# Optimization experiments

Hardware: AMD Instinct MI355X
Metric: run time of the kernel (lower is better)

Reference implementation:

```python
import jax, jax.numpy as jnp
import numpy as np

K_HOP = 2

def _graph_conv(x, A, W, b):
    feats = [x]
    xk = x
    for _ in range(K_HOP):
        xk = jnp.einsum('bmn,bnc->bmc', A, xk)
        feats.append(xk)
    return jnp.concatenate(feats, -1) @ W + b

def _pair_mlp(y, W2, b2, W1, b1, shape):
    # normal_conv: fc1(relu(fc2(y))).reshape(shape)
    return (jax.nn.relu(y @ W2 + b2) @ W1 + b1).reshape(shape)

def setup_inputs():
    key = jax.random.key(0)
    ks = jax.random.split(key, 16)
    B, T, N = 8, 12, 200
    C_IN, H, D, H_ST = 2, 64, 32, 64
    def lin(k, fi, fo):
        k1, k2 = jax.random.split(k)
        s = 1.0 / float(np.sqrt(fi))
        return (jax.random.uniform(k1, (fi, fo), jnp.float32, -s, s),
                jax.random.uniform(k2, (fo,), jnp.float32, -s, s))
    W_s2d, b_s2d = lin(ks[0], H_ST, D)
    W_rz, b_rz = lin(ks[1], 1 + D, 2 * D)
    W_h, b_h = lin(ks[2], 1 + D, D)
    Wc2, bc2 = lin(ks[3], 2 * D, D)
    Wc1, bc1 = lin(ks[4], D, 1)
    Wm2, bm2 = lin(ks[5], 2 * D, D)
    Wm1, bm1 = lin(ks[6], D, 1)
    gin = (C_IN + H) * (1 + K_HOP)
    W_ru, b_ru = lin(ks[7], gin, 2 * H)
    W_cand, b_cand = lin(ks[8], gin, H)
    Wp1, bp1 = lin(ks[9], H, H)
    Wp2, bp2 = lin(ks[10], H, 1)
    x = jax.random.normal(ks[11], (B, T, N, C_IN), jnp.float32)
    node_fea_st = jax.random.normal(ks[12], (N, H_ST), jnp.float32)
    return dict(x=x, node_fea_st=node_fea_st, W_s2d=W_s2d, b_s2d=b_s2d,
                W_rz=W_rz, b_rz=b_rz, W_h=W_h, b_h=b_h,
                Wc2=Wc2, bc2=bc2, Wc1=Wc1, bc1=bc1,
                Wm2=Wm2, bm2=bm2, Wm1=Wm1, bm1=bm1,
                W_ru=W_ru, b_ru=b_ru, W_cand=W_cand, b_cand=b_cand,
                Wp1=Wp1, bp1=bp1, Wp2=Wp2, bp2=bp2)

def reference(x, node_fea_st, W_s2d, b_s2d, W_rz, b_rz, W_h, b_h,
              Wc2, bc2, Wc1, bc1, Wm2, bm2, Wm1, bm1,
              W_ru, b_ru, W_cand, b_cand, Wp1, bp1, Wp2, bp2):
    B, T, N, _ = x.shape
    H = W_cand.shape[1]
    D = W_h.shape[1]
    # states_dy init: linear_s2d(node_fea_st) broadcast over batch
    state_dy0 = jnp.broadcast_to((node_fea_st @ W_s2d + b_s2d)[None], (B, N, D))
    state0 = jnp.zeros((B, N, H), x.dtype)
    xs = jnp.transpose(x, (1, 0, 2, 3))  # [T,B,N,C]

    def step(carry, xt):
        state, state_dy = carry
        inp1 = xt[..., :1]
        # DynamicGraphGRU (conv_method='normal')
        rz = jax.nn.sigmoid(jnp.concatenate([inp1, state_dy], -1) @ W_rz + b_rz)
        r, z = jnp.split(rz, 2, -1)
        h = jnp.tanh(jnp.concatenate([inp1, r * state_dy], -1) @ W_h + b_h)
        new_dy = z * state_dy + (1.0 - z) * h
        s = jax.nn.relu(new_dy)  # [B,N,D]
        y = jnp.concatenate([jnp.broadcast_to(s[:, :, None, :], (B, N, N, D)),
                             jnp.broadcast_to(s[:, None, :, :], (B, N, N, D))], -1)
        g = _pair_mlp(y, Wc2, bc2, Wc1, bc1, (B, N, N))
        m = _pair_mlp(y, Wm2, bm2, Wm1, bm1, (B, N, N))
        A = g * jax.nn.sigmoid(m)  # dynamic graph [B,N,N]
        # DCGRUCell with supports=[A]
        ru = jax.nn.sigmoid(_graph_conv(jnp.concatenate([xt, state], -1), A, W_ru, b_ru))
        rr, u = jnp.split(ru, 2, -1)
        c = jnp.tanh(_graph_conv(jnp.concatenate([xt, rr * state], -1), A, W_cand, b_cand))
        new_state = u * state + (1.0 - u) * c
        return (new_state, new_dy), A

    (state, _), dy_graphs = jax.lax.scan(step, (state0, state_dy0), xs)
    # predictor: Linear -> LeakyReLU -> Linear
    pred = jax.nn.leaky_relu(state @ Wp1 + bp1) @ Wp2 + bp2  # [B,N,1]
    return pred, dy_graphs
```

## Files before the change

kernel.cpp:

```cpp
#include <hip/hip_runtime.h>
#include <math.h>

#define B_ 8
#define T_ 12
#define N_ 200
#define R_ 1600
#define NN_ 40000

__device__ __forceinline__ float sigm(float v) { return 1.f / (1.f + expf(-v)); }

__global__ void __launch_bounds__(256) k_dyall(
        const float* __restrict__ x,  const float* __restrict__ nf,
        const float* __restrict__ Ws2d, const float* __restrict__ bs2d,
        const float* __restrict__ Wrz,  const float* __restrict__ brz,
        const float* __restrict__ Wh,   const float* __restrict__ bh,
        const float* __restrict__ Wc2,  const float* __restrict__ Wm2,
        const float* __restrict__ bc2,  const float* __restrict__ bm2,
        float* __restrict__ Pc, float* __restrict__ Qc,
        float* __restrict__ Pm, float* __restrict__ Qm,
        float* __restrict__ state) {
    __shared__ float sWs2d[64 * 32], sWrz[33 * 64], sWh[33 * 32];
    __shared__ float sWc2[64 * 32], sWm2[64 * 32];
    __shared__ float sbrz[64], sbh[32], sbs2d[32], sbc2[32], sbm2[32];
    __shared__ float nfs[4][64], dy[4][32], in1[4][33], in2[4][33], rz[4][64], s4[4][32];
    int bk = blockIdx.x, tid = threadIdx.x;
    int w = tid >> 6, o = tid & 63;
    int row = bk * 4 + w, b = row / N_, n = row % N_;
    state[bk * 256 + tid] = 0.f;
    for (int idx = tid; idx < 2048; idx += 256) sWs2d[idx] = Ws2d[idx];
    for (int idx = tid; idx < 2112; idx += 256) sWrz[idx] = Wrz[idx];
    for (int idx = tid; idx < 1056; idx += 256) sWh[idx] = Wh[idx];
    for (int idx = tid; idx < 2048; idx += 256) { sWc2[idx] = Wc2[idx]; sWm2[idx] = Wm2[idx]; }
    if (tid < 64) sbrz[tid] = brz[tid];
    if (tid < 32) { sbh[tid] = bh[tid]; sbs2d[tid] = bs2d[tid];
                    sbc2[tid] = bc2[tid]; sbm2[tid] = bm2[tid]; }
    nfs[w][o] = nf[n * 64 + o];
    __syncthreads();
    if (o < 32) {
        float acc = sbs2d[o];
        #pragma unroll 8
        for (int i = 0; i < 64; ++i) acc += nfs[w][i] * sWs2d[i * 32 + o];
        dy[w][o] = acc;
    }
    __syncthreads();
    for (int t = 0; t < T_; ++t) {
        if (o == 0) { float v = x[((b * T_ + t) * N_ + n) * 2]; in1[w][0] = v; in2[w][0] = v; }
        if (o < 32) in1[w][o + 1] = dy[w][o];
        __syncthreads();
        float acc = sbrz[o];
        #pragma unroll
        for (int i = 0; i < 33; ++i) acc += in1[w][i] * sWrz[i * 64 + o];
        rz[w][o] = sigm(acc);
        __syncthreads();
        if (o < 32) in2[w][o + 1] = rz[w][o] * dy[w][o];
        __syncthreads();
        if (o < 32) {
            float h = sbh[o];
            #pragma unroll
            for (int i = 0; i < 33; ++i) h += in2[w][i] * sWh[i * 32 + o];
            h = tanhf(h);
            float z = rz[w][32 + o];
            float nd = z * dy[w][o] + (1.f - z) * h;
            dy[w][o] = nd;
            s4[w][o] = nd > 0.f ? nd : 0.f;
        }
        __syncthreads();
        size_t base = ((size_t)t * R_ + row) * 32;
        for (int idx = o; idx < 128; idx += 64) {
            int mat = idx >> 5, k = idx & 31;
            const float* W = (mat < 2) ? sWc2 : sWm2;
            int rb = (mat & 1) ? 32 : 0;
            float a = (mat == 0) ? sbc2[k] : (mat == 2) ? sbm2[k] : 0.f;
            #pragma unroll
            for (int i = 0; i < 32; ++i) a += s4[w][i] * W[(rb + i) * 32 + k];
            ((mat == 0) ? Pc : (mat == 1) ? Qc : (mat == 2) ? Pm : Qm)[base + k] = a;
        }
        __syncthreads();
    }
}

__global__ void __launch_bounds__(256) k_pairall(
        const float* __restrict__ Pc, const float* __restrict__ Qc,
        const float* __restrict__ Pm, const float* __restrict__ Qm,
        const float* __restrict__ Wc1, const float* __restrict__ bc1,
        const float* __restrict__ Wm1, const float* __restrict__ bm1,
        float* __restrict__ out) {
    __shared__ float sPc[16][36], sQc[16][36], sPm[16][36], sQm[16][36];
    __shared__ float sWc1[32], sWm1[32];
    int z = blockIdx.z;
    int i0 = blockIdx.x * 16, j0 = blockIdx.y * 16;
    int tid = threadIdx.y * 16 + threadIdx.x;
    size_t tb = (size_t)z * N_;
    for (int l = tid; l < 128; l += 256) {
        int r = l >> 3, q = l & 7;
        int gi = i0 + r, gj = j0 + r;
        float4 z4 = make_float4(0.f, 0.f, 0.f, 0.f);
        *(float4*)&sPc[r][4 * q] = (gi < N_) ? *(const float4*)&Pc[(tb + gi) * 32 + 4 * q] : z4;
        *(float4*)&sPm[r][4 * q] = (gi < N_) ? *(const float4*)&Pm[(tb + gi) * 32 + 4 * q] : z4;
        *(float4*)&sQc[r][4 * q] = (gj < N_) ? *(const float4*)&Qc[(tb + gj) * 32 + 4 * q] : z4;
        *(float4*)&sQm[r][4 * q] = (gj < N_) ? *(const float4*)&Qm[(tb + gj) * 32 + 4 * q] : z4;
    }
    if (tid < 32) { sWc1[tid] = Wc1[tid]; sWm1[tid] = Wm1[tid]; }
    __syncthreads();
    int i = i0 + threadIdx.y, j = j0 + threadIdx.x;
    if (i >= N_ || j >= N_) return;
    int ty = threadIdx.y, tx = threadIdx.x;
    float g0 = 0.f, g1 = 0.f, m0 = 0.f, m1 = 0.f;
    #pragma unroll
    for (int kg = 0; kg < 8; ++kg) {
        float4 pc = *(const float4*)&sPc[ty][4 * kg];
        float4 qc = *(const float4*)&sQc[tx][4 * kg];
        float4 wc = *(const float4*)&sWc1[4 * kg];
        g0 += fmaxf(pc.x + qc.x, 0.f) * wc.x + fmaxf(pc.y + qc.y, 0.f) * wc.y;
        g1 += fmaxf(pc.z + qc.z, 0.f) * wc.z + fmaxf(pc.w + qc.w, 0.f) * wc.w;
        float4 pm = *(const float4*)&sPm[ty][4 * kg];
        float4 qm = *(const float4*)&sQm[tx][4 * kg];
        float4 wm = *(const float4*)&sWm1[4 * kg];
        m0 += fmaxf(pm.x + qm.x, 0.f) * wm.x + fmaxf(pm.y + qm.y, 0.f) * wm.y;
        m1 += fmaxf(pm.z + qm.z, 0.f) * wm.z + fmaxf(pm.w + qm.w, 0.f) * wm.w;
    }
    float g = g0 + g1 + bc1[0];
    float m = m0 + m1 + bm1[0];
    out[R_ + (((size_t)z * N_ + i) * N_ + j)] = g * sigm(m);
}

__global__ void __launch_bounds__(256) k_a2(
        const float* __restrict__ Abase, float* __restrict__ Cbase, int nmat) {
    __shared__ float Ast[32][132];
    __shared__ float Bs[32][68];
    int bx = blockIdx.x;
    int z = bx % nmat, tl = bx / nmat;
    int i0 = (tl >> 2) * 128, j0 = (tl & 3) * 64;
    const float* Az = Abase + (size_t)z * NN_;
    float* Cz = Cbase + (size_t)z * NN_;
    int tid = threadIdx.x;
    int tx = tid & 15, ty = tid >> 4;
    float acc[8][4] = {};
    for (int k0 = 0; k0 < 200; k0 += 32) {
        {
            int i = tid >> 1;
            int kb = (tid & 1) * 16;
            int gi = i0 + i;
            #pragma unroll
            for (int q = 0; q < 4; ++q) {
                int k = kb + q * 4;
                int gk = k0 + k;
                float4 v = make_float4(0.f, 0.f, 0.f, 0.f);
                if (gi < N_) {
                    if (gk + 3 < N_) v = *(const float4*)&Az[gi * N_ + gk];
                    else {
                        float t0 = (gk + 0 < N_) ? Az[gi * N_ + gk + 0] : 0.f;
                        float t1 = (gk + 1 < N_) ? Az[gi * N_ + gk + 1] : 0.f;
                        float t2 = (gk + 2 < N_) ? Az[gi * N_ + gk + 2] : 0.f;
                        float t3 = (gk + 3 < N_) ? Az[gi * N_ + gk + 3] : 0.f;
                        v = make_float4(t0, t1, t2, t3);
                    }
                }
                Ast[k + 0][i] = v.x; Ast[k + 1][i] = v.y;
                Ast[k + 2][i] = v.z; Ast[k + 3][i] = v.w;
            }
        }
        {
            #pragma unroll
            for (int q = 0; q < 2; ++q) {
                int id = tid + 256 * q;
                int k = id >> 4, jq = (id & 15) * 4;
                int gk = k0 + k, gj = j0 + jq;
                float4 v = make_float4(0.f, 0.f, 0.f, 0.f);
                if (gk < N_) {
                    if (gj + 3 < N_) v = *(const float4*)&Az[gk * N_ + gj];
                    else {
                        float t0 = (gj + 0 < N_) ? Az[gk * N_ + gj + 0] : 0.f;
                        float t1 = (gj + 1 < N_) ? Az[gk * N_ + gj + 1] : 0.f;
                        float t2 = (gj + 2 < N_) ? Az[gk * N_ + gj + 2] : 0.f;
                        float t3 = (gj + 3 < N_) ? Az[gk * N_ + gj + 3] : 0.f;
                        v = make_float4(t0, t1, t2, t3);
                    }
                }
                *(float4*)&Bs[k][jq] = v;
            }
        }
        __syncthreads();
        #pragma unroll 8
        for (int k = 0; k < 32; ++k) {
            float4 a0 = *(const float4*)&Ast[k][ty * 8];
            float4 a1 = *(const float4*)&Ast[k][ty * 8 + 4];
            float4 bv = *(const float4*)&Bs[k][tx * 4];
            acc[0][0] += a0.x * bv.x; acc[0][1] += a0.x * bv.y; acc[0][2] += a0.x * bv.z; acc[0][3] += a0.x * bv.w;
            acc[1][0] += a0.y * bv.x; acc[1][1] += a0.y * bv.y; acc[1][2] += a0.y * bv.z; acc[1][3] += a0.y * bv.w;
            acc[2][0] += a0.z * bv.x; acc[2][1] += a0.z * bv.y; acc[2][2] += a0.z * bv.z; acc[2][3] += a0.z * bv.w;
            acc[3][0] += a0.w * bv.x; acc[3][1] += a0.w * bv.y; acc[3][2] += a0.w * bv.z; acc[3][3] += a0.w * bv.w;
            acc[4][0] += a1.x * bv.x; acc[4][1] += a1.x * bv.y; acc[4][2] += a1.x * bv.z; acc[4][3] += a1.x * bv.w;
            acc[5][0] += a1.y * bv.x; acc[5][1] += a1.y * bv.y; acc[5][2] += a1.y * bv.z; acc[5][3] += a1.y * bv.w;
            acc[6][0] += a1.z * bv.x; acc[6][1] += a1.z * bv.y; acc[6][2] += a1.z * bv.z; acc[6][3] += a1.z * bv.w;
            acc[7][0] += a1.w * bv.x; acc[7][1] += a1.w * bv.y; acc[7][2] += a1.w * bv.z; acc[7][3] += a1.w * bv.w;
        }
        __syncthreads();
    }
    #pragma unroll
    for (int r = 0; r < 8; ++r) {
        int gi = i0 + ty * 8 + r;
        if (gi >= N_) continue;
        int gj = j0 + tx * 4;
        if (gj + 3 < N_) {
            *(float4*)&Cz[gi * N_ + gj] = make_float4(acc[r][0], acc[r][1], acc[r][2], acc[r][3]);
        } else {
            #pragma unroll
            for (int e = 0; e < 4; ++e) if (gj + e < N_) Cz[gi * N_ + gj + e] = acc[r][e];
        }
    }
}

__global__ void __launch_bounds__(256) k_xh(
        const float* __restrict__ Abase, const float* __restrict__ A2base,
        const float* __restrict__ x, int z0, float* __restrict__ xh) {
    __shared__ float xtl[400];
    int zl = blockIdx.x, tid = threadIdx.x;
    int z = z0 + zl, t = z >> 3, b = z & 7;
    int w = tid >> 6, l = tid & 63;
    const float* xb = x + ((size_t)(b * T_ + t)) * N_ * 2;
    for (int idx = tid; idx < 400; idx += 256) xtl[idx] = xb[idx];
    __syncthreads();
    for (int it = 0; it < 50; ++it) {
        int i = it * 4 + w;
        float p0 = 0.f, p1 = 0.f, p2 = 0.f, p3 = 0.f;
        if (l < 50) {
            float4 a4 = *(const float4*)(Abase + (size_t)zl * NN_ + i * 200 + 4 * l);
            float4 c4 = *(const float4*)(A2base + (size_t)zl * NN_ + i * 200 + 4 * l);
            #pragma unroll
            for (int q = 0; q < 4; ++q) {
                float av = (&a4.x)[q], cv = (&c4.x)[q];
                float x0 = xtl[(4 * l + q) * 2], x1 = xtl[(4 * l + q) * 2 + 1];
                p0 += av * x0; p1 += av * x1; p2 += cv * x0; p3 += cv * x1;
            }
        }
        #pragma unroll
        for (int off = 32; off > 0; off >>= 1) {
            p0 += __shfl_down(p0, off); p1 += __shfl_down(p1, off);
            p2 += __shfl_down(p2, off); p3 += __shfl_down(p3, off);
        }
        if (l == 0) *(float4*)(xh + ((size_t)zl * N_ + i) * 4) = make_float4(p0, p1, p2, p3);
    }
}

__global__ void __launch_bounds__(256) k_ru2(
        const float* __restrict__ At, const float* __restrict__ A2t,
        const float* __restrict__ xht,
        const float* __restrict__ x, int t, const float* __restrict__ state,
        const float* __restrict__ Wru, const float* __restrict__ bru,
        float* __restrict__ rs, float* __restrict__ ub) {
    __shared__ float sF[200 * 64];
    __shared__ float a4s[4 * 200], c4s[4 * 200];
    __shared__ float g8[4 * 132];
    __shared__ float xts[8];
    int bx = blockIdx.x;
    int b = bx & 7, i0 = (bx >> 3) * 4;
    int tid = threadIdx.x;
    {
        const float4* stb = (const float4*)(state + (size_t)b * N_ * 64);
        float4* sFv = (float4*)sF;
        for (int idx = tid; idx < 3200; idx += 256) sFv[idx] = stb[idx];
        const float4* Ar = (const float4*)(At + ((size_t)b * N_ + i0) * 200);
        const float4* Cr = (const float4*)(A2t + ((size_t)b * N_ + i0) * 200);
        float4* av = (float4*)a4s; float4* cv = (float4*)c4s;
        for (int idx = tid; idx < 200; idx += 256) { av[idx] = Ar[idx]; cv[idx] = Cr[idx]; }
        if (tid < 8) xts[tid] = x[((size_t)(b * T_ + t) * N_ + i0 + (tid >> 1)) * 2 + (tid & 1)];
        if (tid >= 8 && tid < 24) {
            int l = tid - 8, rr = l >> 2, q = l & 3;
            g8[rr * 132 + ((q < 2) ? q : q + 64)] = xht[((size_t)b * N_ + i0 + rr) * 4 + q];
        }
    }
    __syncthreads();
    if (tid < 64) {
        int r = tid >> 4, cg = tid & 15;
        const float* ar = a4s + r * 200;
        const float* cr = c4s + r * 200;
        float4 accA = make_float4(0.f, 0.f, 0.f, 0.f);
        float4 accC = make_float4(0.f, 0.f, 0.f, 0.f);
        #pragma unroll 2
        for (int jg = 0; jg < 50; ++jg) {
            float4 a4 = *(const float4*)&ar[4 * jg];
            float4 c4 = *(const float4*)&cr[4 * jg];
            const float* fb = &sF[(4 * jg) * 64 + 4 * cg];
            float4 v0 = *(const float4*)fb;
            float4 v1 = *(const float4*)(fb + 64);
            float4 v2 = *(const float4*)(fb + 128);
            float4 v3 = *(const float4*)(fb + 192);
            accA.x += a4.x * v0.x + a4.y * v1.x + a4.z * v2.x + a4.w * v3.x;
            accA.y += a4.x * v0.y + a4.y * v1.y + a4.z * v2.y + a4.w * v3.y;
            accA.z += a4.x * v0.z + a4.y * v1.z + a4.z * v2.z + a4.w * v3.z;
            accA.w += a4.x * v0.w + a4.y * v1.w + a4.z * v2.w + a4.w * v3.w;
            accC.x += c4.x * v0.x + c4.y * v1.x + c4.z * v2.x + c4.w * v3.x;
            accC.y += c4.x * v0.y + c4.y * v1.y + c4.z * v2.y + c4.w * v3.y;
            accC.z += c4.x * v0.z + c4.y * v1.z + c4.z * v2.z + c4.w * v3.z;
            accC.w += c4.x * v0.w + c4.y * v1.w + c4.z * v2.w + c4.w * v3.w;
        }
        float* gr = &g8[r * 132 + 2 + 4 * cg];
        gr[0] = accA.x; gr[1] = accA.y; gr[2] = accA.z; gr[3] = accA.w;
        float* gr2 = gr + 66;
        gr2[0] = accC.x; gr2[1] = accC.y; gr2[2] = accC.z; gr2[3] = accC.w;
    }
    __syncthreads();
    {
        int c = tid & 127, rq = tid >> 7;
        int r0 = rq * 2, r1 = r0 + 1;
        float bv = bru[c];
        float a0 = bv, a1 = bv;
        #pragma unroll
        for (int k = 0; k < 2; ++k) {
            float wv = Wru[k * 128 + c];
            a0 += xts[r0 * 2 + k] * wv;
            a1 += xts[r1 * 2 + k] * wv;
        }
        #pragma unroll 4
        for (int kg = 0; kg < 16; ++kg) {
            float4 f0 = *(const float4*)&sF[(i0 + r0) * 64 + 4 * kg];
            float4 f1 = *(const float4*)&sF[(i0 + r1) * 64 + 4 * kg];
            const float* Wp = Wru + (2 + 4 * kg) * 128 + c;
            float w0 = Wp[0], w1 = Wp[128], w2 = Wp[256], w3 = Wp[384];
            a0 += f0.x * w0 + f0.y * w1 + f0.z * w2 + f0.w * w3;
            a1 += f1.x * w0 + f1.y * w1 + f1.z * w2 + f1.w * w3;
        }
        #pragma unroll 4
        for (int kg = 0; kg < 33; ++kg) {
            float4 f0 = *(const float4*)&g8[r0 * 132 + 4 * kg];
            float4 f1 = *(const float4*)&g8[r1 * 132 + 4 * kg];
            const float* Wp = Wru + (66 + 4 * kg) * 128 + c;
            float w0 = Wp[0], w1 = Wp[128], w2 = Wp[256], w3 = Wp[384];
            a0 += f0.x * w0 + f0.y * w1 + f0.z * w2 + f0.w * w3;
            a1 += f1.x * w0 + f1.y * w1 + f1.z * w2 + f1.w * w3;
        }
        float v0 = sigm(a0), v1 = sigm(a1);
        size_t gr0 = (size_t)b * N_ + i0 + r0, gr1 = gr0 + 1;
        if (c < 64) {
            rs[gr0 * 64 + c] = v0 * sF[(i0 + r0) * 64 + c];
            rs[gr1 * 64 + c] = v1 * sF[(i0 + r1) * 64 + c];
        } else {
            ub[gr0 * 64 + (c - 64)] = v0;
            ub[gr1 * 64 + (c - 64)] = v1;
        }
    }
}

__global__ void __launch_bounds__(256) k_cand2(
        const float* __restrict__ At, const float* __restrict__ A2t,
        const float* __restrict__ xht,
        const float* __restrict__ x, int t, const float* __restrict__ rsin,
        const float* __restrict__ Wcd, const float* __restrict__ bcd,
        const float* __restrict__ ub, float* __restrict__ state) {
    __shared__ float sF[200 * 64];
    __shared__ float a4s[4 * 200], c4s[4 * 200];
    __shared__ float g8[4 * 132];
    __shared__ float xts[8];
    int bx = blockIdx.x;
    int b = bx & 7, i0 = (bx >> 3) * 4;
    int tid = threadIdx.x;
    {
        const float4* rbv = (const float4*)(rsin + (size_t)b * N_ * 64);
        float4* sFv = (float4*)sF;
        for (int idx = tid; idx < 3200; idx += 256) sFv[idx] = rbv[idx];
        const float4* Ar = (const float4*)(At + ((size_t)b * N_ + i0) * 200);
        const float4* Cr = (const float4*)(A2t + ((size_t)b * N_ + i0) * 200);
        float4* av = (float4*)a4s; float4* cv = (float4*)c4s;
        for (int idx = tid; idx < 200; idx += 256) { av[idx] = Ar[idx]; cv[idx] = Cr[idx]; }
        if (tid < 8) xts[tid] = x[((size_t)(b * T_ + t) * N_ + i0 + (tid >> 1)) * 2 + (tid & 1)];
        if (tid >= 8 && tid < 24) {
            int l = tid - 8, rr = l >> 2, q = l & 3;
            g8[rr * 132 + ((q < 2) ? q : q + 64)] = xht[((size_t)b * N_ + i0 + rr) * 4 + q];
        }
    }
    __syncthreads();
    if (tid < 64) {
        int r = tid >> 4, cg = tid & 15;
        const float* ar = a4s + r * 200;
        const float* cr = c4s + r * 200;
        float4 accA = make_float4(0.f, 0.f, 0.f, 0.f);
        float4 accC = make_float4(0.f, 0.f, 0.f, 0.f);
        #pragma unroll 2
        for (int jg = 0; jg < 50; ++jg) {
            float4 a4 = *(const float4*)&ar[4 * jg];
            float4 c4 = *(const float4*)&cr[4 * jg];
            const float* fb = &sF[(4 * jg) * 64 + 4 * cg];
            float4 v0 = *(const float4*)fb;
            float4 v1 = *(const float4*)(fb + 64);
            float4 v2 = *(const float4*)(fb + 128);
            float4 v3 = *(const float4*)(fb + 192);
            accA.x += a4.x * v0.x + a4.y * v1.x + a4.z * v2.x + a4.w * v3.x;
            accA.y += a4.x * v0.y + a4.y * v1.y + a4.z * v2.y + a4.w * v3.y;
            accA.z += a4.x * v0.z + a4.y * v1.z + a4.z * v2.z + a4.w * v3.z;
            accA.w += a4.x * v0.w + a4.y * v1.w + a4.z * v2.w + a4.w * v3.w;
            accC.x += c4.x * v0.x + c4.y * v1.x + c4.z * v2.x + c4.w * v3.x;
            accC.y += c4.x * v0.y + c4.y * v1.y + c4.z * v2.y + c4.w * v3.y;
            accC.z += c4.x * v0.z + c4.y * v1.z + c4.z * v2.z + c4.w * v3.z;
            accC.w += c4.x * v0.w + c4.y * v1.w + c4.z * v2.w + c4.w * v3.w;
        }
        float* gr = &g8[r * 132 + 2 + 4 * cg];
        gr[0] = accA.x; gr[1] = accA.y; gr[2] = accA.z; gr[3] = accA.w;
        float* gr2 = gr + 66;
        gr2[0] = accC.x; gr2[1] = accC.y; gr2[2] = accC.z; gr2[3] = accC.w;
    }
    __syncthreads();
    {
        int c = tid & 63, r = tid >> 6;
        float a0 = bcd[c];
        #pragma unroll
        for (int k = 0; k < 2; ++k) a0 += xts[r * 2 + k] * Wcd[k * 64 + c];
        #pragma unroll 4
        for (int kg = 0; kg < 16; ++kg) {
            float4 f0 = *(const float4*)&sF[(i0 + r) * 64 + 4 * kg];
            const float* Wp = Wcd + (2 + 4 * kg) * 64 + c;
            a0 += f0.x * Wp[0] + f0.y * Wp[64] + f0.z * Wp[128] + f0.w * Wp[192];
        }
        #pragma unroll 4
        for (int kg = 0; kg < 33; ++kg) {
            float4 f0 = *(const float4*)&g8[r * 132 + 4 * kg];
            const float* Wp = Wcd + (66 + 4 * kg) * 64 + c;
            a0 += f0.x * Wp[0] + f0.y * Wp[64] + f0.z * Wp[128] + f0.w * Wp[192];
        }
        size_t gr = (size_t)b * N_ + i0 + r;
        float cnd = tanhf(a0);
        float u = ub[gr * 64 + c];
        float st = state[gr * 64 + c];
        state[gr * 64 + c] = u * st + (1.f - u) * cnd;
    }
}

__global__ void __launch_bounds__(64) k_pred(
        const float* __restrict__ state,
        const float* __restrict__ Wp1, const float* __restrict__ bp1,
        const float* __restrict__ Wp2, const float* __restrict__ bp2,
        float* __restrict__ out) {
    __shared__ float st[64];
    int row = blockIdx.x;
    int tid = threadIdx.x;
    st[tid] = state[row * 64 + tid];
    __syncthreads();
    float acc = bp1[tid];
    #pragma unroll 8
    for (int a = 0; a < 64; ++a) acc += st[a] * Wp1[a * 64 + tid];
    acc = acc > 0.f ? acc : 0.01f * acc;
    float v = acc * Wp2[tid];
    #pragma unroll
    for (int off = 32; off > 0; off >>= 1) v += __shfl_down(v, off);
    if (tid == 0) out[row] = v + bp2[0];
}

extern "C" void kernel_launch(void* const* d_in, const int* in_sizes, int n_in,
                              void* d_out, int out_size, void* d_ws, size_t ws_size,
                              hipStream_t stream) {
    const float* x    = (const float*)d_in[0];
    const float* nf   = (const float*)d_in[1];
    const float* Ws2d = (const float*)d_in[2];
    const float* bs2d = (const float*)d_in[3];
    const float* Wrz  = (const float*)d_in[4];
    const float* brz  = (const float*)d_in[5];
    const float* Wh   = (const float*)d_in[6];
    const float* bh   = (const float*)d_in[7];
    const float* Wc2  = (const float*)d_in[8];
    const float* bc2  = (const float*)d_in[9];
    const float* Wc1  = (const float*)d_in[10];
    const float* bc1  = (const float*)d_in[11];
    const float* Wm2  = (const float*)d_in[12];
    const float* bm2  = (const float*)d_in[13];
    const float* Wm1  = (const float*)d_in[14];
    const float* bm1  = (const float*)d_in[15];
    const float* Wru  = (const float*)d_in[16];
    const float* bru  = (const float*)d_in[17];
    const float* Wcand= (const float*)d_in[18];
    const float* bcand= (const float*)d_in[19];
    const float* Wp1  = (const float*)d_in[20];
    const float* bp1  = (const float*)d_in[21];
    const float* Wp2  = (const float*)d_in[22];
    const float* bp2  = (const float*)d_in[23];
    float* out = (float*)d_out;

    float* ws = (float*)d_ws;
    const size_t PQ = (size_t)T_ * R_ * 32;
    float* Pc = ws;
    float* Qc = Pc + PQ;
    float* Pm = Qc + PQ;
    float* Qm = Pm + PQ;

    const size_t A2F = (size_t)96 * NN_;
    const size_t XHF = (size_t)96 * N_ * 4;
    const size_t FULL_NEED = (A2F + XHF + 3 * (size_t)R_ * 64) * 4;
    bool full = ws_size >= FULL_NEED;

    const float* Aall = out + R_;

    if (full) {
        float* A2base = ws;
        float* xhbase = ws + A2F;
        float* state  = xhbase + XHF;
        float* rs     = state + (size_t)R_ * 64;
        float* ub     = rs + (size_t)R_ * 64;

        k_dyall<<<400, 256, 0, stream>>>(x, nf, Ws2d, bs2d, Wrz, brz, Wh, bh,
                                         Wc2, Wm2, bc2, bm2, Pc, Qc, Pm, Qm, state);
        k_pairall<<<dim3(13, 13, 96), dim3(16, 16), 0, stream>>>(
            Pc, Qc, Pm, Qm, Wc1, bc1, Wm1, bm1, out);
        k_a2<<<96 * 8, 256, 0, stream>>>(Aall, A2base, 96);
        k_xh<<<96, 256, 0, stream>>>(Aall, A2base, x, 0, xhbase);

        for (int t = 0; t < T_; ++t) {
            const float* At  = Aall + (size_t)t * 8 * NN_;
            const float* A2t = A2base + (size_t)t * 8 * NN_;
            const float* xht = xhbase + (size_t)t * 8 * N_ * 4;
            k_ru2  <<<400, 256, 0, stream>>>(At, A2t, xht, x, t, state, Wru, bru, rs, ub);
            k_cand2<<<400, 256, 0, stream>>>(At, A2t, xht, x, t, rs, Wcand, bcand, ub, state);
        }
        k_pred<<<R_, 64, 0, stream>>>(state, Wp1, bp1, Wp2, bp2, out);
    } else {
        float* A2base = ws + 4 * PQ;
        float* xhbase = A2base + (size_t)8 * NN_;
        float* state  = xhbase + (size_t)8 * N_ * 4;
        float* rs     = state + (size_t)R_ * 64;
        float* ub     = rs + (size_t)R_ * 64;

        k_dyall<<<400, 256, 0, stream>>>(x, nf, Ws2d, bs2d, Wrz, brz, Wh, bh,
                                         Wc2, Wm2, bc2, bm2, Pc, Qc, Pm, Qm, state);
        k_pairall<<<dim3(13, 13, 96), dim3(16, 16), 0, stream>>>(
            Pc, Qc, Pm, Qm, Wc1, bc1, Wm1, bm1, out);
        for (int t = 0; t < T_; ++t) {
            const float* At = Aall + (size_t)t * 8 * NN_;
            k_a2<<<8 * 8, 256, 0, stream>>>(At, A2base, 8);
            k_xh<<<8, 256, 0, stream>>>(At, A2base, x, t * 8, xhbase);
            k_ru2  <<<400, 256, 0, stream>>>(At, A2base, xhbase, x, t, state, Wru, bru, rs, ub);
            k_cand2<<<400, 256, 0, stream>>>(At, A2base, xhbase, x, t, rs, Wcand, bcand, ub, state);
        }
        k_pred<<<R_, 64, 0, stream>>>(state, Wp1, bp1, Wp2, bp2, out);
    }
}
```

Baseline: 561.3 us.

## Restructure GRU graph-conv kernels: 2 rows per block, no LDS state staging

k_ru2 and k_cand2 no longer copy the whole 200x64 per-batch feature matrix into shared memory. Each block now handles 2 rows instead of 4, and the grid doubles to 800 blocks. All four waves share the A/A² contraction by splitting the j range, reducing with cross-lane shuffles and then across waves through shared memory. In k_cand2 the dense projection is also split over two thread halves along K. The intent is to remove the 51KB LDS fill per block, raise occupancy and keep all threads busy instead of one wave. The trade-off is that features are now read from global/L2 many times and extra barriers are added.

```diff
diff --git a/kernel.cpp b/kernel.cpp
--- a/kernel.cpp
+++ b/kernel.cpp
@@ -249,96 +249,86 @@
         const float* __restrict__ x, int t, const float* __restrict__ state,
         const float* __restrict__ Wru, const float* __restrict__ bru,
         float* __restrict__ rs, float* __restrict__ ub) {
-    __shared__ float sF[200 * 64];
-    __shared__ float a4s[4 * 200], c4s[4 * 200];
-    __shared__ float g8[4 * 132];
-    __shared__ float xts[8];
+    __shared__ float a2s[2 * 200], c2s[2 * 200];
+    __shared__ float hpA[4][64], hpC[4][64];
+    __shared__ float g8[2][132];
+    __shared__ float xts[4];
     int bx = blockIdx.x;
-    int b = bx & 7, i0 = (bx >> 3) * 4;
+    int b = bx & 7, i0 = (bx >> 3) * 2;
     int tid = threadIdx.x;
-    {
-        const float4* stb = (const float4*)(state + (size_t)b * N_ * 64);
-        float4* sFv = (float4*)sF;
-        for (int idx = tid; idx < 3200; idx += 256) sFv[idx] = stb[idx];
+    const float* F = state + (size_t)b * (N_ * 64);
+    {
         const float4* Ar = (const float4*)(At + ((size_t)b * N_ + i0) * 200);
         const float4* Cr = (const float4*)(A2t + ((size_t)b * N_ + i0) * 200);
-        float4* av = (float4*)a4s; float4* cv = (float4*)c4s;
-        for (int idx = tid; idx < 200; idx += 256) { av[idx] = Ar[idx]; cv[idx] = Cr[idx]; }
-        if (tid < 8) xts[tid] = x[((size_t)(b * T_ + t) * N_ + i0 + (tid >> 1)) * 2 + (tid & 1)];
-        if (tid >= 8 && tid < 24) {
-            int l = tid - 8, rr = l >> 2, q = l & 3;
-            g8[rr * 132 + ((q < 2) ? q : q + 64)] = xht[((size_t)b * N_ + i0 + rr) * 4 + q];
-        }
-    }
-    __syncthreads();
-    if (tid < 64) {
-        int r = tid >> 4, cg = tid & 15;
-        const float* ar = a4s + r * 200;
-        const float* cr = c4s + r * 200;
+        if (tid < 100) { ((float4*)a2s)[tid] = Ar[tid]; ((float4*)c2s)[tid] = Cr[tid]; }
+        if (tid >= 128 && tid < 132) {
+            int l = tid - 128;
+            xts[l] = x[((size_t)(b * T_ + t) * N_ + i0 + (l >> 1)) * 2 + (l & 1)];
+        }
+        if (tid >= 136 && tid < 144) {
+            int l = tid - 136, rr = l >> 2, q = l & 3;
+            g8[rr][(q < 2) ? q : q + 64] = xht[((size_t)b * N_ + i0 + rr) * 4 + q];
+        }
+    }
+    __syncthreads();
+    {
+        int w = tid >> 6, lane = tid & 63;
+        int r = w & 1, h = w >> 1;
+        int cg = lane & 15, jq = lane >> 4;
+        const float* ar = a2s + r * 200 + h * 100;
+        const float* cr = c2s + r * 200 + h * 100;
+        const float* Fb = F + (size_t)(h * 100) * 64 + 4 * cg;
         float4 accA = make_float4(0.f, 0.f, 0.f, 0.f);
         float4 accC = make_float4(0.f, 0.f, 0.f, 0.f);
-        #pragma unroll 2
-        for (int jg = 0; jg < 50; ++jg) {
-            float4 a4 = *(const float4*)&ar[4 * jg];
-            float4 c4 = *(const float4*)&cr[4 * jg];
-            const float* fb = &sF[(4 * jg) * 64 + 4 * cg];
-            float4 v0 = *(const float4*)fb;
-            float4 v1 = *(const float4*)(fb + 64);
-            float4 v2 = *(const float4*)(fb + 128);
-            float4 v3 = *(const float4*)(fb + 192);
-            accA.x += a4.x * v0.x + a4.y * v1.x + a4.z * v2.x + a4.w * v3.x;
-            accA.y += a4.x * v0.y + a4.y * v1.y + a4.z * v2.y + a4.w * v3.y;
-            accA.z += a4.x * v0.z + a4.y * v1.z + a4.z * v2.z + a4.w * v3.z;
-            accA.w += a4.x * v0.w + a4.y * v1.w + a4.z * v2.w + a4.w * v3.w;
-            accC.x += c4.x * v0.x + c4.y * v1.x + c4.z * v2.x + c4.w * v3.x;
-            accC.y += c4.x * v0.y + c4.y * v1.y + c4.z * v2.y + c4.w * v3.y;
-            accC.z += c4.x * v0.z + c4.y * v1.z + c4.z * v2.z + c4.w * v3.z;
-            accC.w += c4.x * v0.w + c4.y * v1.w + c4.z * v2.w + c4.w * v3.w;
-        }
-        float* gr = &g8[r * 132 + 2 + 4 * cg];
-        gr[0] = accA.x; gr[1] = accA.y; gr[2] = accA.z; gr[3] = accA.w;
-        float* gr2 = gr + 66;
-        gr2[0] = accC.x; gr2[1] = accC.y; gr2[2] = accC.z; gr2[3] = accC.w;
-    }
-    __syncthreads();
-    {
-        int c = tid & 127, rq = tid >> 7;
-        int r0 = rq * 2, r1 = r0 + 1;
-        float bv = bru[c];
-        float a0 = bv, a1 = bv;
-        #pragma unroll
-        for (int k = 0; k < 2; ++k) {
-            float wv = Wru[k * 128 + c];
-            a0 += xts[r0 * 2 + k] * wv;
-            a1 += xts[r1 * 2 + k] * wv;
-        }
+        #pragma unroll 5
+        for (int m = 0; m < 25; ++m) {
+            int j = jq + 4 * m;
+            float av = ar[j], cv = cr[j];
+            float4 f4 = *(const float4*)&Fb[(size_t)j * 64];
+            accA.x += av * f4.x; accA.y += av * f4.y; accA.z += av * f4.z; accA.w += av * f4.w;
+            accC.x += cv * f4.x; accC.y += cv * f4.y; accC.z += cv * f4.z; accC.w += cv * f4.w;
+        }
+        accA.x += __shfl_xor(accA.x, 16); accA.y += __shfl_xor(accA.y, 16);
+        accA.z += __shfl_xor(accA.z, 16); accA.w += __shfl_xor(accA.w, 16);
+        accC.x += __shfl_xor(accC.x, 16); accC.y += __shfl_xor(accC.y, 16);
+        accC.z += __shfl_xor(accC.z, 16); accC.w += __shfl_xor(accC.w, 16);
+        accA.x += __shfl_xor(accA.x, 32); accA.y += __shfl_xor(accA.y, 32);
+        accA.z += __shfl_xor(accA.z, 32); accA.w += __shfl_xor(accA.w, 32);
+        accC.x += __shfl_xor(accC.x, 32); accC.y += __shfl_xor(accC.y, 32);
+        accC.z += __shfl_xor(accC.z, 32); accC.w += __shfl_xor(accC.w, 32);
+        if (lane < 16) {
+            *(float4*)&hpA[w][4 * cg] = accA;
+            *(float4*)&hpC[w][4 * cg] = accC;
+        }
+    }
+    __syncthreads();
+    {
+        int mt = tid >> 7, r = (tid >> 6) & 1, c = tid & 63;
+        float v = mt ? (hpC[r][c] + hpC[2 + r][c]) : (hpA[r][c] + hpA[2 + r][c]);
+        g8[r][(mt ? 68 : 2) + c] = v;
+    }
+    __syncthreads();
+    {
+        int rq = tid >> 7, c = tid & 127;
+        int grow = i0 + rq;
+        const float* Fr = F + (size_t)grow * 64;
+        float a0 = bru[c] + xts[rq * 2 + 0] * Wru[c] + xts[rq * 2 + 1] * Wru[128 + c];
         #pragma unroll 4
         for (int kg = 0; kg < 16; ++kg) {
-            float4 f0 = *(const float4*)&sF[(i0 + r0) * 64 + 4 * kg];
-            float4 f1 = *(const float4*)&sF[(i0 + r1) * 64 + 4 * kg];
-            const float* Wp = Wru + (2 + 4 * kg) * 128 + c;
-            float w0 = Wp[0], w1 = Wp[128], w2 = Wp[256], w3 = Wp[384];
-            a0 += f0.x * w0 + f0.y * w1 + f0.z * w2 + f0.w * w3;
-            a1 += f1.x * w0 + f1.y * w1 + f1.z * w2 + f1.w * w3;
+            float4 f0 = *(const float4*)&Fr[4 * kg];
+            const float* Wp = Wru + (size_t)(2 + 4 * kg) * 128 + c;
+            a0 += f0.x * Wp[0] + f0.y * Wp[128] + f0.z * Wp[256] + f0.w * Wp[384];
         }
         #pragma unroll 4
         for (int kg = 0; kg < 33; ++kg) {
-            float4 f0 = *(const float4*)&g8[r0 * 132 + 4 * kg];
-            float4 f1 = *(const float4*)&g8[r1 * 132 + 4 * kg];
-            const float* Wp = Wru + (66 + 4 * kg) * 128 + c;
-            float w0 = Wp[0], w1 = Wp[128], w2 = Wp[256], w3 = Wp[384];
-            a0 += f0.x * w0 + f0.y * w1 + f0.z * w2 + f0.w * w3;
-            a1 += f1.x * w0 + f1.y * w1 + f1.z * w2 + f1.w * w3;
-        }
-        float v0 = sigm(a0), v1 = sigm(a1);
-        size_t gr0 = (size_t)b * N_ + i0 + r0, gr1 = gr0 + 1;
-        if (c < 64) {
-            rs[gr0 * 64 + c] = v0 * sF[(i0 + r0) * 64 + c];
-            rs[gr1 * 64 + c] = v1 * sF[(i0 + r1) * 64 + c];
-        } else {
-            ub[gr0 * 64 + (c - 64)] = v0;
-            ub[gr1 * 64 + (c - 64)] = v1;
-        }
+            float4 f0 = *(const float4*)&g8[rq][4 * kg];
+            const float* Wp = Wru + (size_t)(66 + 4 * kg) * 128 + c;
+            a0 += f0.x * Wp[0] + f0.y * Wp[128] + f0.z * Wp[256] + f0.w * Wp[384];
+        }
+        float v = sigm(a0);
+        size_t go = (size_t)b * N_ + grow;
+        if (c < 64) rs[go * 64 + c] = v * Fr[c];
+        else        ub[go * 64 + (c - 64)] = v;
     }
 }
 
@@ -348,80 +338,104 @@
         const float* __restrict__ x, int t, const float* __restrict__ rsin,
         const float* __restrict__ Wcd, const float* __restrict__ bcd,
         const float* __restrict__ ub, float* __restrict__ state) {
-    __shared__ float sF[200 * 64];
-    __shared__ float a4s[4 * 200], c4s[4 * 200];
-    __shared__ float g8[4 * 132];
-    __shared__ float xts[8];
+    __shared__ float a2s[2 * 200], c2s[2 * 200];
+    __shared__ float hpA[4][64], hpC[4][64];
+    __shared__ float g8[2][132];
+    __shared__ float xts[4];
+    __shared__ float gp[2][2][64];
     int bx = blockIdx.x;
-    int b = bx & 7, i0 = (bx >> 3) * 4;
+    int b = bx & 7, i0 = (bx >> 3) * 2;
     int tid = threadIdx.x;
-    {
-        const float4* rbv = (const float4*)(rsin + (size_t)b * N_ * 64);
-        float4* sFv = (float4*)sF;
-        for (int idx = tid; idx < 3200; idx += 256) sFv[idx] = rbv[idx];
+    const float* F = rsin + (size_t)b * (N_ * 64);
+    {
         const float4* Ar = (const float4*)(At + ((size_t)b * N_ + i0) * 200);
         const float4* Cr = (const float4*)(A2t + ((size_t)b * N_ + i0) * 200);
-        float4* av = (float4*)a4s; float4* cv = (float4*)c4s;
-        for (int idx = tid; idx < 200; idx += 256) { av[idx] = Ar[idx]; cv[idx] = Cr[idx]; }
-        if (tid < 8) xts[tid] = x[((size_t)(b * T_ + t) * N_ + i0 + (tid >> 1)) * 2 + (tid & 1)];
-        if (tid >= 8 && tid < 24) {
-            int l = tid - 8, rr = l >> 2, q = l & 3;
-            g8[rr * 132 + ((q < 2) ? q : q + 64)] = xht[((size_t)b * N_ + i0 + rr) * 4 + q];
-        }
-    }
-    __syncthreads();
-    if (tid < 64) {
-        int r = tid >> 4, cg = tid & 15;
-        const float* ar = a4s + r * 200;
-        const float* cr = c4s + r * 200;
+        if (tid < 100) { ((float4*)a2s)[tid] = Ar[tid]; ((float4*)c2s)[tid] = Cr[tid]; }
+        if (tid >= 128 && tid < 132) {
+            int l = tid - 128;
+            xts[l] = x[((size_t)(b * T_ + t) * N_ + i0 + (l >> 1)) * 2 + (l & 1)];
+        }
+        if (tid >= 136 && tid < 144) {
+            int l = tid - 136, rr = l >> 2, q = l & 3;
+            g8[rr][(q < 2) ? q : q + 64] = xht[((size_t)b * N_ + i0 + rr) * 4 + q];
+        }
+    }
+    __syncthreads();
+    {
+        int w = tid >> 6, lane = tid & 63;
+        int r = w & 1, h = w >> 1;
+        int cg = lane & 15, jq = lane >> 4;
+        const float* ar = a2s + r * 200 + h * 100;
+        const float* cr = c2s + r * 200 + h * 100;
+        const float* Fb = F + (size_t)(h * 100) * 64 + 4 * cg;
         float4 accA = make_float4(0.f, 0.f, 0.f, 0.f);
         float4 accC = make_float4(0.f, 0.f, 0.f, 0.f);
-        #pragma unroll 2
-        for (int jg = 0; jg < 50; ++jg) {
-            float4 a4 = *(const float4*)&ar[4 * jg];
-            float4 c4 = *(const float4*)&cr[4 * jg];
-            const float* fb = &sF[(4 * jg) * 64 + 4 * cg];
-            float4 v0 = *(const float4*)fb;
-            float4 v1 = *(const float4*)(fb + 64);
-            float4 v2 = *(const float4*)(fb + 128);
-            float4 v3 = *(const float4*)(fb + 192);
-            accA.x += a4.x * v0.x + a4.y * v1.x + a4.z * v2.x + a4.w * v3.x;
-            accA.y += a4.x * v0.y + a4.y * v1.y + a4.z * v2.y + a4.w * v3.y;
-            accA.z += a4.x * v0.z + a4.y * v1.z + a4.z * v2.z + a4.w * v3.z;
-            accA.w += a4.x * v0.w + a4.y * v1.w + a4.z * v2.w + a4.w * v3.w;
-            accC.x += c4.x * v0.x + c4.y * v1.x + c4.z * v2.x + c4.w * v3.x;
-            accC.y += c4.x * v0.y + c4.y * v1.y + c4.z * v2.y + c4.w * v3.y;
-            accC.z += c4.x * v0.z + c4.y * v1.z + c4.z * v2.z + c4.w * v3.z;
-            accC.w += c4.x * v0.w + c4.y * v1.w + c4.z * v2.w + c4.w * v3.w;
-        }
-        float* gr = &g8[r * 132 + 2 + 4 * cg];
-        gr[0] = accA.x; gr[1] = accA.y; gr[2] = accA.z; gr[3] = accA.w;
-        float* gr2 = gr + 66;
-        gr2[0] = accC.x; gr2[1] = accC.y; gr2[2] = accC.z; gr2[3] = accC.w;
-    }
-    __syncthreads();
-    {
-        int c = tid & 63, r = tid >> 6;
-        float a0 = bcd[c];
-        #pragma unroll
-        for (int k = 0; k < 2; ++k) a0 += xts[r * 2 + k] * Wcd[k * 64 + c];
-        #pragma unroll 4
-        for (int kg = 0; kg < 16; ++kg) {
-            float4 f0 = *(const float4*)&sF[(i0 + r) * 64 + 4 * kg];
-            const float* Wp = Wcd + (2 + 4 * kg) * 64 + c;
-            a0 += f0.x * Wp[0] + f0.y * Wp[64] + f0.z * Wp[128] + f0.w * Wp[192];
-        }
-        #pragma unroll 4
-        for (int kg = 0; kg < 33; ++kg) {
-            float4 f0 = *(const float4*)&g8[r * 132 + 4 * kg];
-            const float* Wp = Wcd + (66 + 4 * kg) * 64 + c;
-            a0 += f0.x * Wp[0] + f0.y * Wp[64] + f0.z * Wp[128] + f0.w * Wp[192];
-        }
-        size_t gr = (size_t)b * N_ + i0 + r;
-        float cnd = tanhf(a0);
-        float u = ub[gr * 64 + c];
-        float st = state[gr * 64 + c];
-        state[gr * 64 + c] = u * st + (1.f - u) * cnd;
+        #pragma unroll 5
+        for (int m = 0; m < 25; ++m) {
+            int j = jq + 4 * m;
+            float av = ar[j], cv = cr[j];
+            float4 f4 = *(const float4*)&Fb[(size_t)j * 64];
+            accA.x += av * f4.x; accA.y += av * f4.y; accA.z += av * f4.z; accA.w += av * f4.w;
+            accC.x += cv * f4.x; accC.y += cv * f4.y; accC.z += cv * f4.z; accC.w += cv * f4.w;
+        }
+        accA.x += __shfl_xor(accA.x, 16); accA.y += __shfl_xor(accA.y, 16);
+        accA.z += __shfl_xor(accA.z, 16); accA.w += __shfl_xor(accA.w, 16);
+        accC.x += __shfl_xor(accC.x, 16); accC.y += __shfl_xor(accC.y, 16);
+        accC.z += __shfl_xor(accC.z, 16); accC.w += __shfl_xor(accC.w, 16);
+        accA.x += __shfl_xor(accA.x, 32); accA.y += __shfl_xor(accA.y, 32);
+        accA.z += __shfl_xor(accA.z, 32); accA.w += __shfl_xor(accA.w, 32);
+        accC.x += __shfl_xor(accC.x, 32); accC.y += __shfl_xor(accC.y, 32);
+        accC.z += __shfl_xor(accC.z, 32); accC.w += __shfl_xor(accC.w, 32);
+        if (lane < 16) {
+            *(float4*)&hpA[w][4 * cg] = accA;
+            *(float4*)&hpC[w][4 * cg] = accC;
+        }
+    }
+    __syncthreads();
+    {
+        int mt = tid >> 7, r = (tid >> 6) & 1, c = tid & 63;
+        float v = mt ? (hpC[r][c] + hpC[2 + r][c]) : (hpA[r][c] + hpA[2 + r][c]);
+        g8[r][(mt ? 68 : 2) + c] = v;
+    }
+    __syncthreads();
+    {
+        int kh = tid >> 7, rq = (tid >> 6) & 1, c = tid & 63;
+        int grow = i0 + rq;
+        const float* Fr = F + (size_t)grow * 64;
+        float a0 = 0.f;
+        if (kh == 0) {
+            a0 = bcd[c] + xts[rq * 2 + 0] * Wcd[c] + xts[rq * 2 + 1] * Wcd[64 + c];
+            #pragma unroll 4
+            for (int kg = 0; kg < 16; ++kg) {
+                float4 f0 = *(const float4*)&Fr[4 * kg];
+                const float* Wp = Wcd + (size_t)(2 + 4 * kg) * 64 + c;
+                a0 += f0.x * Wp[0] + f0.y * Wp[64] + f0.z * Wp[128] + f0.w * Wp[192];
+            }
+            #pragma unroll 4
+            for (int kg = 0; kg < 8; ++kg) {
+                float4 f0 = *(const float4*)&g8[rq][4 * kg];
+                const float* Wp = Wcd + (size_t)(66 + 4 * kg) * 64 + c;
+                a0 += f0.x * Wp[0] + f0.y * Wp[64] + f0.z * Wp[128] + f0.w * Wp[192];
+            }
+        } else {
+            #pragma unroll 5
+            for (int kg = 8; kg < 33; ++kg) {
+                float4 f0 = *(const float4*)&g8[rq][4 * kg];
+                const float* Wp = Wcd + (size_t)(66 + 4 * kg) * 64 + c;
+                a0 += f0.x * Wp[0] + f0.y * Wp[64] + f0.z * Wp[128] + f0.w * Wp[192];
+            }
+        }
+        gp[kh][rq][c] = a0;
+    }
+    __syncthreads();
+    if (tid < 128) {
+        int rq = tid >> 6, c = tid & 63;
+        size_t go = (size_t)b * N_ + i0 + rq;
+        float a = gp[0][rq][c] + gp[1][rq][c];
+        float cnd = tanhf(a);
+        float u = ub[go * 64 + c];
+        float st = state[go * 64 + c];
+        state[go * 64 + c] = u * st + (1.f - u) * cnd;
     }
 }
 
@@ -506,8 +520,8 @@
             const float* At  = Aall + (size_t)t * 8 * NN_;
             const float* A2t = A2base + (size_t)t * 8 * NN_;
             const float* xht = xhbase + (size_t)t * 8 * N_ * 4;
-            k_ru2  <<<400, 256, 0, stream>>>(At, A2t, xht, x, t, state, Wru, bru, rs, ub);
-            k_cand2<<<400, 256, 0, stream>>>(At, A2t, xht, x, t, rs, Wcand, bcand, ub, state);
+            k_ru2  <<<800, 256, 0, stream>>>(At, A2t, xht, x, t, state, Wru, bru, rs, ub);
+            k_cand2<<<800, 256, 0, stream>>>(At, A2t, xht, x, t, rs, Wcand, bcand, ub, state);
         }
         k_pred<<<R_, 64, 0, stream>>>(state, Wp1, bp1, Wp2, bp2, out);
     } else {
@@ -525,8 +539,8 @@
             const float* At = Aall + (size_t)t * 8 * NN_;
             k_a2<<<8 * 8, 256, 0, stream>>>(At, A2base, 8);
             k_xh<<<8, 256, 0, stream>>>(At, A2base, x, t * 8, xhbase);
-            k_ru2  <<<400, 256, 0, stream>>>(At, A2base, xhbase, x, t, state, Wru, bru, rs, ub);
-            k_cand2<<<400, 256, 0, stream>>>(At, A2base, xhbase, x, t, rs, Wcand, bcand, ub, state);
+            k_ru2  <<<800, 256, 0, stream>>>(At, A2base, xhbase, x, t, state, Wru, bru, rs, ub);
+            k_cand2<<<800, 256, 0, stream>>>(At, A2base, xhbase, x, t, rs, Wcand, bcand, ub, state);
         }
         k_pred<<<R_, 64, 0, stream>>>(state, Wp1, bp1, Wp2, bp2, out);
     }
```

Measured after the change: 550.8 us. Within noise of the previous version (-1.9%).
